# Performance work log

Hardware: AMD Instinct MI355X
Metric: run time of the kernel (lower is better)

## Reference

```python
import jax, jax.numpy as jnp
import numpy as np

B, S, D, H, DH, F = 2, 2048, 1024, 16, 64, 4096
K = 2048  # number of selected tokens (capacity_gamma=0.5 of B*S)
EPS = 1e-6
ROPE_THETA = 10000.0


def setup_inputs() -> dict:
    key = jax.random.key(0)
    ks = jax.random.split(key, 12)
    w = lambda k, shp: jax.random.normal(k, shp, dtype=jnp.float32) * 0.02
    # K unique flat indices into the B*S token grid (every other token -> unique, sorted)
    sel_flat = jnp.arange(K, dtype=jnp.int64) * 2
    return {
        "hidden_states": jax.random.normal(ks[0], (B, S, D), dtype=jnp.float32),
        "gating_signal": jax.random.uniform(ks[1], (B, S), dtype=jnp.float32),
        "sel_flat": sel_flat,
        "position_ids": jnp.tile(jnp.arange(S, dtype=jnp.int64), (B, 1)),
        "ln1_w": jnp.ones((D,), jnp.float32),
        "ln2_w": jnp.ones((D,), jnp.float32),
        "wq": w(ks[2], (D, H * DH)), "bq": jnp.zeros((H * DH,), jnp.float32),
        "wk": w(ks[3], (D, H * DH)), "bk": jnp.zeros((H * DH,), jnp.float32),
        "wv": w(ks[4], (D, H * DH)), "bv": jnp.zeros((H * DH,), jnp.float32),
        "wo": w(ks[5], (H * DH, D)),
        "w_gate": w(ks[6], (D, F)),
        "w_up": w(ks[7], (D, F)),
        "w_down": w(ks[8], (F, D)),
    }


def _rmsnorm(x, w):
    var = jnp.mean(jnp.square(x), axis=-1, keepdims=True)
    return x * jax.lax.rsqrt(var + EPS) * w


def _rope(x, pos):
    # x: [K, H, DH], pos: [K]
    half = DH // 2
    inv_freq = 1.0 / (ROPE_THETA ** (jnp.arange(half, dtype=jnp.float32) / half))
    ang = pos.astype(jnp.float32)[:, None] * inv_freq  # [K, half]
    cos = jnp.cos(ang)[:, None, :]
    sin = jnp.sin(ang)[:, None, :]
    x1, x2 = x[..., :half], x[..., half:]
    return jnp.concatenate([x1 * cos - x2 * sin, x2 * cos + x1 * sin], axis=-1)


def reference(hidden_states, gating_signal, sel_flat, position_ids,
              ln1_w, ln2_w, wq, bq, wk, bk, wv, bv, wo, w_gate, w_up, w_down):
    b_idx = sel_flat // S
    t_idx = sel_flat % S

    # --- gather selected tokens ---
    x = hidden_states[b_idx, t_idx]          # [K, D]
    g = gating_signal[b_idx, t_idx]          # [K]
    pos = position_ids[b_idx, t_idx]         # [K]

    # --- Qwen2 block on the selected tokens (single sequence of length K) ---
    h = _rmsnorm(x, ln1_w)
    q = _rope((h @ wq + bq).reshape(K, H, DH), pos)
    k = _rope((h @ wk + bk).reshape(K, H, DH), pos)
    v = (h @ wv + bv).reshape(K, H, DH)

    scores = jnp.einsum("qhd,khd->hqk", q, k) / np.sqrt(DH)  # [H, K, K]
    causal = jnp.tril(jnp.ones((K, K), dtype=bool))
    scores = jnp.where(causal, scores, jnp.finfo(scores.dtype).min)
    probs = jax.nn.softmax(scores, axis=-1)
    attn = jnp.einsum("hqk,khd->qhd", probs, v).reshape(K, H * DH) @ wo

    x1 = x + attn
    h2 = _rmsnorm(x1, ln2_w)
    mlp = (jax.nn.silu(h2 @ w_gate) * (h2 @ w_up)) @ w_down
    y = x1 + mlp                              # processed tokens [K, D]

    # --- gated residual scatter-back ---
    updated = x + (y - x) * g[:, None]
    return hidden_states.at[b_idx, t_idx].set(updated)
```

## Files before the change

### kernel.cpp

```cpp
#include <hip/hip_runtime.h>
#include <hip/hip_bf16.h>
#include <stdint.h>

#define K_TOK 2048
#define D_DIM 1024
#define H_N   16
#define DH_N  64
#define F_DIM 4096
#define S_SEQ 2048

typedef __attribute__((ext_vector_type(4))) float f32x4;
typedef __attribute__((ext_vector_type(8))) short bf16x8;

__device__ __forceinline__ float bf2f(ushort u) {
  union { unsigned u; float f; } c; c.u = ((unsigned)u) << 16; return c.f;
}
__device__ __forceinline__ ushort f2bf(float f) {
  union { float f; unsigned u; } c; c.f = f;
  unsigned x = c.u + 0x7fffu + ((c.u >> 16) & 1u);
  return (ushort)(x >> 16);
}

#define GLOAD_LDS16(GP, LP)                                                   \
  __builtin_amdgcn_global_load_lds(                                           \
      (const __attribute__((address_space(1))) unsigned int*)(GP),            \
      (__attribute__((address_space(3))) unsigned int*)(LP), 16, 0, 0)

__global__ __launch_bounds__(256) void prep_all(
    const float* __restrict__ wq, const float* __restrict__ wk,
    const float* __restrict__ wv, const float* __restrict__ wo,
    const float* __restrict__ wg, const float* __restrict__ wu,
    const float* __restrict__ wd, const float* __restrict__ bq,
    const float* __restrict__ bk, const float* __restrict__ bv,
    ushort* __restrict__ qkvT, ushort* __restrict__ woT,
    ushort* __restrict__ guT, ushort* __restrict__ wdT,
    float* __restrict__ biasqkv) {
  __shared__ float tile[64][65];
  int b = blockIdx.x;
  if (b >= 4096) {
    int i = (b - 4096) * 256 + threadIdx.x;
    if (i < 3072)
      biasqkv[i] = (i < 1024) ? bq[i] : (i < 2048 ? bk[i - 1024] : bv[i - 2048]);
    return;
  }
  const float* src;
  ushort* dst;
  int C, mul, add, ldd, tid_tile;
  if (b < 1024) {
    int seg = b >> 8; tid_tile = b & 255; C = 1024; mul = 1; add = 0; ldd = 1024;
    if (seg == 0) { src = wq; dst = qkvT; }
    else if (seg == 1) { src = wk; dst = qkvT + 1024 * 1024; }
    else if (seg == 2) { src = wv; dst = qkvT + 2048 * 1024; }
    else { src = wo; dst = woT; }
  } else if (b < 2048) { src = wg; dst = guT; tid_tile = b - 1024; C = 4096; mul = 2; add = 0; ldd = 1024; }
  else if (b < 3072) { src = wu; dst = guT; tid_tile = b - 2048; C = 4096; mul = 2; add = 1; ldd = 1024; }
  else { src = wd; dst = wdT; tid_tile = b - 3072; C = 1024; mul = 1; add = 0; ldd = 4096; }

  int nbx = C >> 6;
  int bx = tid_tile % nbx, by = tid_tile / nbx;
  int c0 = bx << 6, r0 = by << 6;
  int tx = threadIdx.x & 15, ty = threadIdx.x >> 4;
#pragma unroll
  for (int i = 0; i < 4; ++i) {
    float4 v = *(const float4*)&src[(size_t)(r0 + ty + i * 16) * C + c0 + tx * 4];
    *(float4*)&tile[ty + i * 16][tx * 4] = v;
  }
  __syncthreads();
#pragma unroll
  for (int i = 0; i < 4; ++i) {
    int c = ty + i * 16;
    ushort4 o;
    o.x = f2bf(tile[tx * 4 + 0][c]);
    o.y = f2bf(tile[tx * 4 + 1][c]);
    o.z = f2bf(tile[tx * 4 + 2][c]);
    o.w = f2bf(tile[tx * 4 + 3][c]);
    *(ushort4*)&dst[(size_t)((c0 + c) * mul + add) * ldd + r0 + tx * 4] = o;
  }
}

__global__ __launch_bounds__(256) void gather_copy(
    const float* __restrict__ hs, const float* __restrict__ gating,
    const int* __restrict__ sel32, const int* __restrict__ pos32,
    const float* __restrict__ w, float* __restrict__ outc,
    float* __restrict__ xbuf, ushort* __restrict__ hbuf,
    float* __restrict__ gbuf, int* __restrict__ rowb, int* __restrict__ rowt,
    int* __restrict__ rowpos) {
  __shared__ float red[4];
  int tid = threadIdx.x;
  if (blockIdx.x < 4096) {
    int idx = blockIdx.x * 256 + tid;
    ((float4*)outc)[idx] = ((const float4*)hs)[idx];
    return;
  }
  int i = blockIdx.x - 4096;
  bool is64 = (sel32[1] == 0 && sel32[3] == 0 && sel32[5] == 0);
  int sel = is64 ? sel32[2 * i] : sel32[i];
  int b = sel >> 11;
  int t = sel & 2047;
  const float4* src = (const float4*)(hs + ((size_t)b * S_SEQ + t) * D_DIM);
  float4 v = src[tid];
  float ss = v.x * v.x + v.y * v.y + v.z * v.z + v.w * v.w;
  for (int off = 32; off; off >>= 1) ss += __shfl_xor(ss, off);
  if ((tid & 63) == 0) red[tid >> 6] = ss;
  __syncthreads();
  float tot = red[0] + red[1] + red[2] + red[3];
  float rms = rsqrtf(tot * (1.f / 1024.f) + 1e-6f);
  ((float4*)(xbuf + (size_t)i * D_DIM))[tid] = v;
  float4 lw = ((const float4*)w)[tid];
  ushort4 hv;
  hv.x = f2bf(v.x * rms * lw.x); hv.y = f2bf(v.y * rms * lw.y);
  hv.z = f2bf(v.z * rms * lw.z); hv.w = f2bf(v.w * rms * lw.w);
  *(ushort4*)&hbuf[(size_t)i * D_DIM + tid * 4] = hv;
  if (tid == 0) {
    rowb[i] = b; rowt[i] = t;
    bool is64p = (pos32[1] == 0 && pos32[3] == 0 && pos32[5] == 0);
    int pidx = b * S_SEQ + t;
    rowpos[i] = is64p ? pos32[2 * pidx] : pos32[pidx];
    gbuf[i] = gating[pidx];
  }
}

__global__ __launch_bounds__(256) void rmsnorm_ep1(const float* __restrict__ xbuf,
                                                   const float* __restrict__ pb,
                                                   const float* __restrict__ w,
                                                   float* __restrict__ x1out,
                                                   ushort* __restrict__ h2out) {
  int i = blockIdx.x, tid = threadIdx.x;
  __shared__ float red[4];
  size_t e = (size_t)i * D_DIM;
  float4 v = ((const float4*)(xbuf + e))[tid];
  float4 p0 = ((const float4*)(pb + e))[tid];
  float4 p1 = ((const float4*)(pb + 2097152 + e))[tid];
  v.x += p0.x + p1.x; v.y += p0.y + p1.y; v.z += p0.z + p1.z; v.w += p0.w + p1.w;
  ((float4*)(x1out + e))[tid] = v;
  float ss = v.x * v.x + v.y * v.y + v.z * v.z + v.w * v.w;
  for (int off = 32; off; off >>= 1) ss += __shfl_xor(ss, off);
  if ((tid & 63) == 0) red[tid >> 6] = ss;
  __syncthreads();
  float tot = red[0] + red[1] + red[2] + red[3];
  float rms = rsqrtf(tot * (1.f / 1024.f) + 1e-6f);
  float4 lw = ((const float4*)w)[tid];
  ushort4 hv;
  hv.x = f2bf(v.x * rms * lw.x); hv.y = f2bf(v.y * rms * lw.y);
  hv.z = f2bf(v.z * rms * lw.z); hv.w = f2bf(v.w * rms * lw.w);
  *(ushort4*)&h2out[e + tid * 4] = hv;
}

__global__ __launch_bounds__(256) void ep3_k(const float* __restrict__ pb,
                                             const float* __restrict__ x1b,
                                             const float* __restrict__ xbuf,
                                             const float* __restrict__ gbuf,
                                             const int* __restrict__ rowb,
                                             const int* __restrict__ rowt,
                                             float* __restrict__ out) {
  int idx = blockIdx.x * 256 + threadIdx.x;
  int row = idx >> 8, c4 = idx & 255;
  size_t e = (size_t)row * D_DIM + c4 * 4;
  float4 s0 = *(const float4*)(pb + e);
  float4 s1 = *(const float4*)(pb + 2097152 + e);
  float4 s2 = *(const float4*)(pb + 2 * 2097152 + e);
  float4 s3 = *(const float4*)(pb + 3 * 2097152 + e);
  float4 x = *(const float4*)(xbuf + e);
  float4 x1 = *(const float4*)(x1b + e);
  float g = gbuf[row];
  float4 r;
  r.x = x.x + (x1.x + s0.x + s1.x + s2.x + s3.x - x.x) * g;
  r.y = x.y + (x1.y + s0.y + s1.y + s2.y + s3.y - x.y) * g;
  r.z = x.z + (x1.z + s0.z + s1.z + s2.z + s3.z - x.z) * g;
  r.w = x.w + (x1.w + s0.w + s1.w + s2.w + s3.w - x.w) * g;
  *(float4*)(out + ((size_t)rowb[row] * S_SEQ + rowt[row]) * D_DIM + c4 * 4) = r;
}

template <int MODE>
__global__ __launch_bounds__(256) void gemm_bt(
    const ushort* __restrict__ A, const ushort* __restrict__ BT,
    int M, int N, int ldk, int kdeff, int per,
    const float* __restrict__ bias,
    ushort* __restrict__ outb, float* __restrict__ outf) {
  __shared__ ushort lA[2][128 * 64];
  __shared__ ushort lB[2][128 * 64];
  int tid = threadIdx.x;
  int lane = tid & 63, wid = tid >> 6;
  int kidx = blockIdx.x / per;
  int bid = blockIdx.x % per;
  int nbn = N >> 7;
  int tm = bid / nbn, tn = bid % nbn;
  int wr = wid >> 1, wc = wid & 1;
  f32x4 acc[4][4];
#pragma unroll
  for (int m = 0; m < 4; ++m)
#pragma unroll
    for (int n = 0; n < 4; ++n) acc[m][n] = (f32x4){0.f, 0.f, 0.f, 0.f};

  const ushort* Ab = A + (size_t)(tm * 128) * ldk + (size_t)kidx * kdeff;
  const ushort* Bb = BT + (size_t)(tn * 128) * ldk + (size_t)kidx * kdeff;
  int lr = lane & 15, lg = lane >> 4;
  int prow = lane >> 3;
  int pch = lane & 7;
  int nk = kdeff >> 6;

  auto STG = [&](int bi, int t) {
#pragma unroll
    for (int p = 0; p < 4; ++p) {
      int rb = p * 32 + wid * 8;
      int row = rb + prow;
      int g = pch ^ (row & 7);
      GLOAD_LDS16(Ab + (size_t)row * ldk + t * 64 + g * 8, &lA[bi][rb * 64]);
      GLOAD_LDS16(Bb + (size_t)row * ldk + t * 64 + g * 8, &lB[bi][rb * 64]);
    }
  };

  STG(0, 0);
  STG(1, 1);
  asm volatile("s_waitcnt vmcnt(8)" ::: "memory");
  __builtin_amdgcn_s_barrier();

  for (int t = 0; t < nk; ++t) {
    int c = t & 1;
    const char* bA = (const char*)&lA[c][0];
    const char* bB = (const char*)&lB[c][0];
    bf16x8 bfv[4][2], af[4];
#pragma unroll
    for (int n = 0; n < 4; ++n) {
      int row = wc * 64 + n * 16 + lr;
#pragma unroll
      for (int kk = 0; kk < 2; ++kk)
        bfv[n][kk] = *(const bf16x8*)(bB + row * 128 + ((kk * 64 + lg * 16) ^ ((row & 7) << 4)));
    }
#pragma unroll
    for (int m = 0; m < 4; ++m) {
      int row = wr * 64 + m * 16 + lr;
      af[m] = *(const bf16x8*)(bA + row * 128 + ((lg * 16) ^ ((row & 7) << 4)));
    }
    __builtin_amdgcn_s_setprio(1);
#pragma unroll
    for (int m = 0; m < 4; ++m)
#pragma unroll
      for (int n = 0; n < 4; ++n)
        acc[m][n] = __builtin_amdgcn_mfma_f32_16x16x32_bf16(af[m], bfv[n][0], acc[m][n], 0, 0, 0);
    __builtin_amdgcn_s_setprio(0);
#pragma unroll
    for (int m = 0; m < 4; ++m) {
      int row = wr * 64 + m * 16 + lr;
      af[m] = *(const bf16x8*)(bA + row * 128 + ((64 + lg * 16) ^ ((row & 7) << 4)));
    }
    asm volatile("s_waitcnt lgkmcnt(0)" ::: "memory");
    __builtin_amdgcn_s_barrier();
    if (t + 2 < nk) STG(c, t + 2);
    __builtin_amdgcn_sched_barrier(0);
    __builtin_amdgcn_s_setprio(1);
#pragma unroll
    for (int m = 0; m < 4; ++m)
#pragma unroll
      for (int n = 0; n < 4; ++n)
        acc[m][n] = __builtin_amdgcn_mfma_f32_16x16x32_bf16(af[m], bfv[n][1], acc[m][n], 0, 0, 0);
    __builtin_amdgcn_s_setprio(0);
    if (t < nk - 1) {
      if (t + 2 < nk)
        asm volatile("s_waitcnt vmcnt(8)" ::: "memory");
      else
        asm volatile("s_waitcnt vmcnt(0)" ::: "memory");
      __builtin_amdgcn_s_barrier();
    }
  }

#pragma unroll
  for (int m = 0; m < 4; ++m) {
#pragma unroll
    for (int n = 0; n < 4; ++n) {
#pragma unroll
      for (int r = 0; r < 4; ++r) {
        int gr = tm * 128 + wr * 64 + m * 16 + lg * 4 + r;
        int gc = tn * 128 + wc * 64 + n * 16 + lr;
        float val = acc[m][n][r];
        if (MODE == 0) {
          outb[(size_t)gr * N + gc] = f2bf(val + bias[gc]);
        } else {
          outf[((size_t)kidx * M + gr) * N + gc] = val;
        }
      }
    }
  }
}

__global__ __launch_bounds__(512, 2) void gemm256_gu(const ushort* __restrict__ A,
                                                     const ushort* __restrict__ BT,
                                                     ushort* __restrict__ outb) {
  __shared__ ushort lA[2][256 * 64];
  __shared__ ushort lB[2][256 * 64];
  int tid = threadIdx.x, lane = tid & 63, wid = tid >> 6;
  int bid = blockIdx.x;
  int tn = (bid & 7) * 4 + ((bid >> 3) & 3);
  int tm = bid >> 5;
  int wm = wid >> 2, wn = wid & 3;
  int lr = lane & 15, lg = lane >> 4;
  const ushort* Ab = A + (size_t)(tm * 256) * 1024;
  const ushort* Bb = BT + (size_t)(tn * 256) * 1024;

  f32x4 acc[8][4];
#pragma unroll
  for (int m = 0; m < 8; ++m)
#pragma unroll
    for (int n = 0; n < 4; ++n) acc[m][n] = (f32x4){0.f, 0.f, 0.f, 0.f};

  int grow = lane >> 3;
  int gsw = (lane & 7) ^ grow;

  auto STG = [&](int bi, int t) {
#pragma unroll
    for (int r = 0; r < 4; ++r) {
      int rb = wid * 4 + r;
      int row = rb * 8 + grow;
      GLOAD_LDS16(Ab + (size_t)row * 1024 + t * 64 + gsw * 8, &lA[bi][rb * 512]);
      GLOAD_LDS16(Bb + (size_t)row * 1024 + t * 64 + gsw * 8, &lB[bi][rb * 512]);
    }
  };

  STG(0, 0);
  STG(1, 1);
  asm volatile("s_waitcnt vmcnt(8)" ::: "memory");
  __builtin_amdgcn_s_barrier();

  for (int t = 0; t < 16; ++t) {
    int c = t & 1;
    const char* bA = (const char*)&lA[c][0];
    const char* bB = (const char*)&lB[c][0];
    bf16x8 bfr[4][2], afh[4][2];
#pragma unroll
    for (int n = 0; n < 4; ++n) {
      int row = wn * 64 + n * 16 + lr;
#pragma unroll
      for (int kk = 0; kk < 2; ++kk)
        bfr[n][kk] = *(const bf16x8*)(bB + row * 128 + ((kk * 64 + lg * 16) ^ ((lr & 7) << 4)));
    }
#pragma unroll
    for (int m = 0; m < 4; ++m) {
      int row = wm * 128 + m * 16 + lr;
#pragma unroll
      for (int kk = 0; kk < 2; ++kk)
        afh[m][kk] = *(const bf16x8*)(bA + row * 128 + ((kk * 64 + lg * 16) ^ ((lr & 7) << 4)));
    }
    __builtin_amdgcn_s_setprio(1);
#pragma unroll
    for (int m = 0; m < 4; ++m)
#pragma unroll
      for (int n = 0; n < 4; ++n)
#pragma unroll
        for (int kk = 0; kk < 2; ++kk)
          acc[m][n] = __builtin_amdgcn_mfma_f32_16x16x32_bf16(afh[m][kk], bfr[n][kk],
                                                              acc[m][n], 0, 0, 0);
    __builtin_amdgcn_s_setprio(0);
#pragma unroll
    for (int m = 0; m < 4; ++m) {
      int row = wm * 128 + 64 + m * 16 + lr;
#pragma unroll
      for (int kk = 0; kk < 2; ++kk)
        afh[m][kk] = *(const bf16x8*)(bA + row * 128 + ((kk * 64 + lg * 16) ^ ((lr & 7) << 4)));
    }
    asm volatile("s_waitcnt lgkmcnt(0)" ::: "memory");
    __builtin_amdgcn_s_barrier();
    if (t + 2 < 16) STG(c, t + 2);
    __builtin_amdgcn_sched_barrier(0);
    __builtin_amdgcn_s_setprio(1);
#pragma unroll
    for (int m = 0; m < 4; ++m)
#pragma unroll
      for (int n = 0; n < 4; ++n)
#pragma unroll
        for (int kk = 0; kk < 2; ++kk)
          acc[4 + m][n] = __builtin_amdgcn_mfma_f32_16x16x32_bf16(afh[m][kk], bfr[n][kk],
                                                                  acc[4 + m][n], 0, 0, 0);
    __builtin_amdgcn_s_setprio(0);
    if (t < 15) {
      if (t + 2 < 16)
        asm volatile("s_waitcnt vmcnt(8)" ::: "memory");
      else
        asm volatile("s_waitcnt vmcnt(0)" ::: "memory");
      __builtin_amdgcn_s_barrier();
    }
  }

#pragma unroll
  for (int m = 0; m < 8; ++m) {
#pragma unroll
    for (int n = 0; n < 4; ++n) {
#pragma unroll
      for (int r = 0; r < 4; ++r) {
        int gr = tm * 256 + wm * 128 + m * 16 + lg * 4 + r;
        int gc = tn * 256 + wn * 64 + n * 16 + lr;
        float val = acc[m][n][r];
        float other = __shfl_xor(val, 1);
        if (!(lane & 1)) {
          float g = val, u = other;
          float a = g / (1.f + __expf(-g)) * u;
          outb[(size_t)gr * (F_DIM) + (gc >> 1)] = f2bf(a);
        }
      }
    }
  }
}

__global__ __launch_bounds__(256) void rope_vtrans(const ushort* __restrict__ qkv,
                                                   const int* __restrict__ rowpos,
                                                   ushort* __restrict__ qr,
                                                   ushort* __restrict__ kr,
                                                   ushort* __restrict__ vt) {
  __shared__ ushort tile[32][33];
  if (blockIdx.x < 4096) {
    int idx = blockIdx.x * 256 + threadIdx.x;
    int i = idx >> 9;
    int rem = idx & 511;
    int h = rem >> 5, d = rem & 31;
    float pos = (float)rowpos[i];
    float inv = __expf(-(float)d * (9.210340371976184f / 32.0f));
    float ang = pos * inv;
    float sn, cs;
    __sincosf(ang, &sn, &cs);
    size_t base = (size_t)i * 3072;
    float q1 = bf2f(qkv[base + h * 64 + d]);
    float q2 = bf2f(qkv[base + h * 64 + 32 + d]);
    float k1 = bf2f(qkv[base + 1024 + h * 64 + d]);
    float k2 = bf2f(qkv[base + 1024 + h * 64 + 32 + d]);
    size_t ob = ((size_t)h * K_TOK + i) * DH_N;
    qr[ob + d] = f2bf((q1 * cs - q2 * sn) * 0.125f);
    qr[ob + 32 + d] = f2bf((q2 * cs + q1 * sn) * 0.125f);
    kr[ob + d] = f2bf(k1 * cs - k2 * sn);
    kr[ob + 32 + d] = f2bf(k2 * cs + k1 * sn);
    return;
  }
  int bid = blockIdx.x - 4096;
  int bx = bid & 63, by = bid >> 6;
  int i0 = bx << 5, c0 = by << 5;
  int tx = threadIdx.x & 31, ty = threadIdx.x >> 5;
#pragma unroll
  for (int j = 0; j < 32; j += 8)
    tile[ty + j][tx] = qkv[(size_t)(i0 + ty + j) * 3072 + 2048 + c0 + tx];
  __syncthreads();
#pragma unroll
  for (int j = 0; j < 32; j += 8)
    vt[(size_t)(c0 + ty + j) * K_TOK + i0 + tx] = tile[tx][ty + j];
}

__global__ __launch_bounds__(256) void attn_mfma(const ushort* __restrict__ qr,
                                                 const ushort* __restrict__ kr,
                                                 const ushort* __restrict__ vt,
                                                 ushort* __restrict__ ows,
                                                 float* __restrict__ mlws) {
  __shared__ ushort ktile[2][64 * 64];
  __shared__ ushort vtile[2][64 * 64];
  __shared__ ushort pbuf[4][16 * 64];
  int tid = threadIdx.x, lane = tid & 63, wid = tid >> 6;
  int bid = blockIdx.x;
  int h = bid / 144;
  int rem = 143 - (bid % 144);
  int g = 0;
  while (rem >= 2 * (g + 1) * (g + 2)) ++g;
  int rem2 = rem - 2 * g * (g + 1);
  int qt = (g << 2) + rem2 / (g + 1);
  int ci = rem2 % (g + 1);
  int slot = h * 144 + rem;
  int q0 = qt << 6;
  int t0 = ci << 2;
  int t1 = min(t0 + 3, qt);

  const ushort* Kh = kr + (size_t)h * K_TOK * DH_N;
  const ushort* Vh = vt + (size_t)h * DH_N * K_TOK;
  int lr = lane & 15, lg = lane >> 4;
  int qbase = q0 + wid * 16;

  bf16x8 qf[2];
  const ushort* Qp = qr + ((size_t)h * K_TOK + qbase + lr) * DH_N + lg * 8;
  qf[0] = *(const bf16x8*)(Qp);
  qf[1] = *(const bf16x8*)(Qp + 32);

  f32x4 oa[4];
  float mreg[4], lreg[4];
#pragma unroll
  for (int ct = 0; ct < 4; ++ct) oa[ct] = (f32x4){0.f, 0.f, 0.f, 0.f};
#pragma unroll
  for (int r = 0; r < 4; ++r) { mreg[r] = -1e30f; lreg[r] = 0.f; }

  char* pws = (char*)&pbuf[wid][0];
  int srow8 = lane >> 3, schunk = lane & 7;

  auto stage = [&](int bi, int kb) {
#pragma unroll
    for (int j = 0; j < 2; ++j) {
      int rbase = wid * 16 + j * 8;
      int row = rbase + srow8;
      int gch = schunk ^ (row & 7);
      GLOAD_LDS16(Kh + (size_t)(kb + row) * DH_N + gch * 8, &ktile[bi][rbase * 64]);
      GLOAD_LDS16(Vh + (size_t)row * K_TOK + kb + gch * 8, &vtile[bi][rbase * 64]);
    }
  };

  stage(0, t0 << 6);
  int cur = 0;
  for (int t = t0; t <= t1; ++t) {
    int kb = t << 6;
    __syncthreads();
    if (t < t1) stage(cur ^ 1, (t + 1) << 6);

    const char* kt = (const char*)&ktile[cur][0];
    const char* vtl = (const char*)&vtile[cur][0];

    f32x4 sa[4];
#pragma unroll
    for (int ct = 0; ct < 4; ++ct) sa[ct] = (f32x4){0.f, 0.f, 0.f, 0.f};
#pragma unroll
    for (int s = 0; s < 2; ++s) {
#pragma unroll
      for (int ct = 0; ct < 4; ++ct) {
        int row = ct * 16 + lr;
        bf16x8 kf = *(const bf16x8*)(kt + row * 128 + ((s * 64 + lg * 16) ^ ((row & 7) << 4)));
        sa[ct] = __builtin_amdgcn_mfma_f32_16x16x32_bf16(qf[s], kf, sa[ct], 0, 0, 0);
      }
    }

#pragma unroll
    for (int r = 0; r < 4; ++r) {
      int q = qbase + lg * 4 + r;
      int prow = lg * 4 + r;
      float sv[4];
      float mx = mreg[r];
#pragma unroll
      for (int ct = 0; ct < 4; ++ct) {
        int key = kb + ct * 16 + lr;
        float x = sa[ct][r];
        sv[ct] = (key <= q) ? x : -1e30f;
        mx = fmaxf(mx, sv[ct]);
      }
      mx = fmaxf(mx, __shfl_xor(mx, 1));
      mx = fmaxf(mx, __shfl_xor(mx, 2));
      mx = fmaxf(mx, __shfl_xor(mx, 4));
      mx = fmaxf(mx, __shfl_xor(mx, 8));
      float resc = __expf(mreg[r] - mx);
      float ps = 0.f;
#pragma unroll
      for (int ct = 0; ct < 4; ++ct) {
        float p = __expf(sv[ct] - mx);
        ps += p;
        *(ushort*)(pws + prow * 128 + ((ct * 32 + lr * 2) ^ ((prow & 7) << 4))) = f2bf(p);
      }
      ps += __shfl_xor(ps, 1);
      ps += __shfl_xor(ps, 2);
      ps += __shfl_xor(ps, 4);
      ps += __shfl_xor(ps, 8);
      lreg[r] = lreg[r] * resc + ps;
      mreg[r] = mx;
#pragma unroll
      for (int ct = 0; ct < 4; ++ct) oa[ct][r] *= resc;
    }

    bf16x8 pf[2];
#pragma unroll
    for (int s = 0; s < 2; ++s)
      pf[s] = *(const bf16x8*)(pws + lr * 128 + ((s * 64 + lg * 16) ^ ((lr & 7) << 4)));
#pragma unroll
    for (int s = 0; s < 2; ++s) {
#pragma unroll
      for (int ct = 0; ct < 4; ++ct) {
        int row = ct * 16 + lr;
        bf16x8 vf = *(const bf16x8*)(vtl + row * 128 + ((s * 64 + lg * 16) ^ ((row & 7) << 4)));
        oa[ct] = __builtin_amdgcn_mfma_f32_16x16x32_bf16(pf[s], vf, oa[ct], 0, 0, 0);
      }
    }
    cur ^= 1;
  }

#pragma unroll
  for (int ct = 0; ct < 4; ++ct) {
#pragma unroll
    for (int r = 0; r < 4; ++r) {
      int prow = wid * 16 + lg * 4 + r;
      ows[(size_t)slot * 4096 + prow * 64 + ct * 16 + lr] = f2bf(oa[ct][r]);
    }
  }
  if (lr == 0) {
#pragma unroll
    for (int r = 0; r < 4; ++r) {
      int prow = wid * 16 + lg * 4 + r;
      mlws[(size_t)slot * 128 + prow] = mreg[r];
      mlws[(size_t)slot * 128 + 64 + prow] = lreg[r];
    }
  }
}

__global__ __launch_bounds__(256) void attn_combine(const ushort* __restrict__ ows,
                                                    const float* __restrict__ mlws,
                                                    ushort* __restrict__ aout) {
  int bid = blockIdx.x;
  int h = bid & 15, qt = bid >> 4;
  int g = qt >> 2;
  int nc = g + 1;
  int base = h * 144 + 2 * g * (g + 1) + (qt & 3) * nc;
  int tid = threadIdx.x;
  int row = tid >> 2, c0 = (tid & 3) * 16;
  float M = -1e30f;
  for (int i = 0; i < nc; ++i)
    M = fmaxf(M, mlws[(size_t)(base + i) * 128 + row]);
  float L = 0.f;
  float acc[16];
#pragma unroll
  for (int j = 0; j < 16; ++j) acc[j] = 0.f;
  for (int i = 0; i < nc; ++i) {
    size_t sl = (size_t)(base + i);
    float w = __expf(mlws[sl * 128 + row] - M);
    L += mlws[sl * 128 + 64 + row] * w;
    const bf16x8* op = (const bf16x8*)(ows + sl * 4096 + row * 64 + c0);
    bf16x8 v0 = op[0], v1 = op[1];
#pragma unroll
    for (int j = 0; j < 8; ++j) acc[j] += bf2f(((ushort)v0[j])) * w;
#pragma unroll
    for (int j = 0; j < 8; ++j) acc[8 + j] += bf2f(((ushort)v1[j])) * w;
  }
  float inv = 1.f / L;
  int q = qt * 64 + row;
  ushort* dst = aout + (size_t)q * D_DIM + h * DH_N + c0;
#pragma unroll
  for (int j = 0; j < 16; ++j) dst[j] = f2bf(acc[j] * inv);
}

extern "C" void kernel_launch(void* const* d_in, const int* in_sizes, int n_in,
                              void* d_out, int out_size, void* d_ws, size_t ws_size,
                              hipStream_t stream) {
  const float* hs = (const float*)d_in[0];
  const float* gating = (const float*)d_in[1];
  const int* sel32 = (const int*)d_in[2];
  const int* pos32 = (const int*)d_in[3];
  const float* ln1w = (const float*)d_in[4];
  const float* ln2w = (const float*)d_in[5];
  const float* wq = (const float*)d_in[6];
  const float* bq = (const float*)d_in[7];
  const float* wk = (const float*)d_in[8];
  const float* bk = (const float*)d_in[9];
  const float* wv = (const float*)d_in[10];
  const float* bv = (const float*)d_in[11];
  const float* wo = (const float*)d_in[12];
  const float* wg = (const float*)d_in[13];
  const float* wu = (const float*)d_in[14];
  const float* wd = (const float*)d_in[15];
  float* out = (float*)d_out;

  char* wsb = (char*)d_ws;
  size_t off = 0;
  auto alloc = [&](size_t bytes) -> void* {
    void* p = wsb + off;
    off += (bytes + 255) & ~(size_t)255;
    return p;
  };
  ushort* qkvT = (ushort*)alloc(3072ull * 1024 * 2);
  ushort* woT = (ushort*)alloc(1024ull * 1024 * 2);
  ushort* guT = (ushort*)alloc(8192ull * 1024 * 2);
  ushort* wdT = (ushort*)alloc(1024ull * 4096 * 2);
  float* biasqkv = (float*)alloc(3072 * 4);
  float* xbuf = (float*)alloc(2048ull * 1024 * 4);
  ushort* hbuf = (ushort*)alloc(2048ull * 1024 * 2);
  ushort* qkv = (ushort*)alloc(2048ull * 3072 * 2);
  ushort* qrb = (ushort*)alloc(16ull * 2048 * 64 * 2);
  ushort* krb = (ushort*)alloc(16ull * 2048 * 64 * 2);
  ushort* vtb = (ushort*)alloc(16ull * 64 * 2048 * 2);
  ushort* aoutb = (ushort*)alloc(2048ull * 1024 * 2);
  float* pbuf = (float*)hbuf;
  float* x1b = (float*)alloc(2048ull * 1024 * 4);
  ushort* h2b = (ushort*)alloc(2048ull * 1024 * 2);
  ushort* actb = (ushort*)alloc(2048ull * 4096 * 2);
  ushort* aows = (ushort*)x1b;
  float* amlws = (float*)((char*)x1b + 2304ull * 4096 * 2);
  float* gbuf = (float*)alloc(2048 * 4);
  int* rowb = (int*)alloc(2048 * 4);
  int* rowt = (int*)alloc(2048 * 4);
  int* rowpos = (int*)alloc(2048 * 4);
  if (off > ws_size) return;

  prep_all<<<4108, 256, 0, stream>>>(wq, wk, wv, wo, wg, wu, wd, bq, bk, bv, qkvT, woT, guT,
                                     wdT, biasqkv);
  gather_copy<<<6144, 256, 0, stream>>>(hs, gating, sel32, pos32, ln1w, out, xbuf, hbuf, gbuf,
                                        rowb, rowt, rowpos);
  gemm_bt<0><<<16 * 24, 256, 0, stream>>>(hbuf, qkvT, 2048, 3072, 1024, 1024, 16 * 24, biasqkv,
                                          qkv, nullptr);
  rope_vtrans<<<6144, 256, 0, stream>>>(qkv, rowpos, qrb, krb, vtb);
  attn_mfma<<<16 * 144, 256, 0, stream>>>(qrb, krb, vtb, aows, amlws);
  attn_combine<<<512, 256, 0, stream>>>(aows, amlws, aoutb);
  gemm_bt<4><<<2 * 16 * 8, 256, 0, stream>>>(aoutb, woT, 2048, 1024, 1024, 512, 16 * 8, nullptr,
                                             nullptr, pbuf);
  rmsnorm_ep1<<<2048, 256, 0, stream>>>(xbuf, pbuf, ln2w, x1b, h2b);
  gemm256_gu<<<256, 512, 0, stream>>>(h2b, guT, actb);
  gemm_bt<4><<<4 * 16 * 8, 256, 0, stream>>>(actb, wdT, 2048, 1024, 4096, 1024, 16 * 8, nullptr,
                                             nullptr, pbuf);
  ep3_k<<<2048, 256, 0, stream>>>(pbuf, x1b, xbuf, gbuf, rowb, rowt, out);
}
```

Measured before the change: 194.9 us.

## Switch gate/up GEMM to triple-buffered K=32 stages with packed LDS layout

The fused gate/up GEMM previously staged K=64 slices in two LDS buffers. It now stages K=32 slices in three buffers, packing two matrix rows per 128-byte LDS row with an XOR swizzle. Loads are issued two stages ahead, with an extra barrier pair per iteration. This uses less LDS per stage and adds pipeline depth, but doubles the loop iterations and barrier count and issues fewer MFMAs per synchronisation.

New measurement: 206.1 us. 5.7% more time.

```diff
diff --git a/kernel.cpp b/kernel.cpp
--- a/kernel.cpp
+++ b/kernel.cpp
@@ -286,8 +286,8 @@
 __global__ __launch_bounds__(512, 2) void gemm256_gu(const ushort* __restrict__ A,
                                                      const ushort* __restrict__ BT,
                                                      ushort* __restrict__ outb) {
-  __shared__ ushort lA[2][256 * 64];
-  __shared__ ushort lB[2][256 * 64];
+  __shared__ ushort lA[3][128 * 64];
+  __shared__ ushort lB[3][128 * 64];
   int tid = threadIdx.x, lane = tid & 63, wid = tid >> 6;
   int bid = blockIdx.x;
   int tn = (bid & 7) * 4 + ((bid >> 3) & 3);
@@ -303,81 +303,66 @@
 #pragma unroll
     for (int n = 0; n < 4; ++n) acc[m][n] = (f32x4){0.f, 0.f, 0.f, 0.f};
 
-  int grow = lane >> 3;
-  int gsw = (lane & 7) ^ grow;
+  int sR0 = wid * 8 + (lane >> 3);
+  int scp = lane & 7;
 
   auto STG = [&](int bi, int t) {
 #pragma unroll
-    for (int r = 0; r < 4; ++r) {
-      int rb = wid * 4 + r;
-      int row = rb * 8 + grow;
-      GLOAD_LDS16(Ab + (size_t)row * 1024 + t * 64 + gsw * 8, &lA[bi][rb * 512]);
-      GLOAD_LDS16(Bb + (size_t)row * 1024 + t * 64 + gsw * 8, &lB[bi][rb * 512]);
+    for (int j = 0; j < 2; ++j) {
+      int R = j * 64 + sR0;
+      int c = scp ^ (R & 7);
+      int grow = 2 * R + (c >> 2);
+      int kch = c & 3;
+      GLOAD_LDS16(Ab + (size_t)grow * 1024 + t * 32 + kch * 8, &lA[bi][(j * 64 + wid * 8) * 64]);
+      GLOAD_LDS16(Bb + (size_t)grow * 1024 + t * 32 + kch * 8, &lB[bi][(j * 64 + wid * 8) * 64]);
     }
   };
 
   STG(0, 0);
   STG(1, 1);
+  STG(2, 2);
   asm volatile("s_waitcnt vmcnt(8)" ::: "memory");
   __builtin_amdgcn_s_barrier();
 
-  for (int t = 0; t < 16; ++t) {
-    int c = t & 1;
-    const char* bA = (const char*)&lA[c][0];
-    const char* bB = (const char*)&lB[c][0];
-    bf16x8 bfr[4][2], afh[4][2];
+  for (int t = 0; t < 32; ++t) {
+    if (t > 0) {
+      __builtin_amdgcn_s_barrier();
+      __builtin_amdgcn_sched_barrier(0);
+      if (t + 2 < 32) {
+        STG((t + 2) % 3, t + 2);
+        asm volatile("s_waitcnt vmcnt(8)" ::: "memory");
+      } else if (t + 1 < 32) {
+        asm volatile("s_waitcnt vmcnt(4)" ::: "memory");
+      } else {
+        asm volatile("s_waitcnt vmcnt(0)" ::: "memory");
+      }
+      __builtin_amdgcn_s_barrier();
+      __builtin_amdgcn_sched_barrier(0);
+    }
+    const char* bA = (const char*)&lA[t % 3][0];
+    const char* bB = (const char*)&lB[t % 3][0];
+    bf16x8 bf[4], af[8];
 #pragma unroll
     for (int n = 0; n < 4; ++n) {
-      int row = wn * 64 + n * 16 + lr;
-#pragma unroll
-      for (int kk = 0; kk < 2; ++kk)
-        bfr[n][kk] = *(const bf16x8*)(bB + row * 128 + ((kk * 64 + lg * 16) ^ ((lr & 7) << 4)));
-    }
-#pragma unroll
-    for (int m = 0; m < 4; ++m) {
-      int row = wm * 128 + m * 16 + lr;
-#pragma unroll
-      for (int kk = 0; kk < 2; ++kk)
-        afh[m][kk] = *(const bf16x8*)(bA + row * 128 + ((kk * 64 + lg * 16) ^ ((lr & 7) << 4)));
+      int rho = wn * 64 + n * 16 + lr;
+      int R = rho >> 1;
+      int cc = ((rho & 1) * 4 + lg) ^ (R & 7);
+      bf[n] = *(const bf16x8*)(bB + R * 128 + cc * 16);
+    }
+#pragma unroll
+    for (int m = 0; m < 8; ++m) {
+      int rho = wm * 128 + m * 16 + lr;
+      int R = rho >> 1;
+      int cc = ((rho & 1) * 4 + lg) ^ (R & 7);
+      af[m] = *(const bf16x8*)(bA + R * 128 + cc * 16);
     }
     __builtin_amdgcn_s_setprio(1);
 #pragma unroll
-    for (int m = 0; m < 4; ++m)
+    for (int m = 0; m < 8; ++m)
 #pragma unroll
       for (int n = 0; n < 4; ++n)
-#pragma unroll
-        for (int kk = 0; kk < 2; ++kk)
-          acc[m][n] = __builtin_amdgcn_mfma_f32_16x16x32_bf16(afh[m][kk], bfr[n][kk],
-                                                              acc[m][n], 0, 0, 0);
+        acc[m][n] = __builtin_amdgcn_mfma_f32_16x16x32_bf16(af[m], bf[n], acc[m][n], 0, 0, 0);
     __builtin_amdgcn_s_setprio(0);
-#pragma unroll
-    for (int m = 0; m < 4; ++m) {
-      int row = wm * 128 + 64 + m * 16 + lr;
-#pragma unroll
-      for (int kk = 0; kk < 2; ++kk)
-        afh[m][kk] = *(const bf16x8*)(bA + row * 128 + ((kk * 64 + lg * 16) ^ ((lr & 7) << 4)));
-    }
-    asm volatile("s_waitcnt lgkmcnt(0)" ::: "memory");
-    __builtin_amdgcn_s_barrier();
-    if (t + 2 < 16) STG(c, t + 2);
-    __builtin_amdgcn_sched_barrier(0);
-    __builtin_amdgcn_s_setprio(1);
-#pragma unroll
-    for (int m = 0; m < 4; ++m)
-#pragma unroll
-      for (int n = 0; n < 4; ++n)
-#pragma unroll
-        for (int kk = 0; kk < 2; ++kk)
-          acc[4 + m][n] = __builtin_amdgcn_mfma_f32_16x16x32_bf16(afh[m][kk], bfr[n][kk],
-                                                                  acc[4 + m][n], 0, 0, 0);
-    __builtin_amdgcn_s_setprio(0);
-    if (t < 15) {
-      if (t + 2 < 16)
-        asm volatile("s_waitcnt vmcnt(8)" ::: "memory");
-      else
-        asm volatile("s_waitcnt vmcnt(0)" ::: "memory");
-      __builtin_amdgcn_s_barrier();
-    }
   }
 
 #pragma unroll
```

## Restructure gate-up GEMM into 8-wave ping-pong phases with split-K half tiles

Applied to the files above, without the earlier changes.

Rewrites the main loop of the fused gate/up GEMM kernel. Each 64-wide K tile now splits into two 32-wide halves, each stored in its own LDS buffer with a new paired-row XOR swizzle. Each iteration runs four barrier-separated phases, and the global->LDS loads for the next tile (A half, then B half) are interleaved between MFMA clusters. The aim is finer-grained overlap of loads with MFMA, in the style of a ping-pong schedule, plus fewer registers held for fragments. The cost is more barriers per iteration and a new swizzle layout that has to stay correct.

After: 202.5 us. 3.9% more time.

```diff
diff --git a/kernel.cpp b/kernel.cpp
--- a/kernel.cpp
+++ b/kernel.cpp
@@ -286,8 +286,8 @@
 __global__ __launch_bounds__(512, 2) void gemm256_gu(const ushort* __restrict__ A,
                                                      const ushort* __restrict__ BT,
                                                      ushort* __restrict__ outb) {
-  __shared__ ushort lA[2][256 * 64];
-  __shared__ ushort lB[2][256 * 64];
+  __shared__ ushort lA[2][2][128 * 64];
+  __shared__ ushort lB[2][2][128 * 64];
   int tid = threadIdx.x, lane = tid & 63, wid = tid >> 6;
   int bid = blockIdx.x;
   int tn = (bid & 7) * 4 + ((bid >> 3) & 3);
@@ -303,82 +303,142 @@
 #pragma unroll
     for (int n = 0; n < 4; ++n) acc[m][n] = (f32x4){0.f, 0.f, 0.f, 0.f};
 
-  int grow = lane >> 3;
-  int gsw = (lane & 7) ^ grow;
-
-  auto STG = [&](int bi, int t) {
-#pragma unroll
-    for (int r = 0; r < 4; ++r) {
-      int rb = wid * 4 + r;
-      int row = rb * 8 + grow;
-      GLOAD_LDS16(Ab + (size_t)row * 1024 + t * 64 + gsw * 8, &lA[bi][rb * 512]);
-      GLOAD_LDS16(Bb + (size_t)row * 1024 + t * 64 + gsw * 8, &lB[bi][rb * 512]);
+  int sR = lane >> 3;
+  int scp = lane & 7;
+
+  auto STG_A = [&](int buf, int t, int kk) {
+#pragma unroll
+    for (int j = 0; j < 2; ++j) {
+      int R = j * 64 + wid * 8 + sR;
+      int c = scp ^ (R & 7);
+      int grow = 2 * R + (c >> 2);
+      GLOAD_LDS16(Ab + (size_t)grow * 1024 + t * 64 + kk * 32 + (c & 3) * 8,
+                  &lA[buf][kk][(j * 64 + wid * 8) * 64]);
     }
   };
-
-  STG(0, 0);
-  STG(1, 1);
-  asm volatile("s_waitcnt vmcnt(8)" ::: "memory");
-  __builtin_amdgcn_s_barrier();
+  auto STG_B = [&](int buf, int t, int kk) {
+#pragma unroll
+    for (int j = 0; j < 2; ++j) {
+      int R = j * 64 + wid * 8 + sR;
+      int c = scp ^ (R & 7);
+      int grow = 2 * R + (c >> 2);
+      GLOAD_LDS16(Bb + (size_t)grow * 1024 + t * 64 + kk * 32 + (c & 3) * 8,
+                  &lB[buf][kk][(j * 64 + wid * 8) * 64]);
+    }
+  };
+
+#define PH_BAR() { __builtin_amdgcn_s_barrier(); __builtin_amdgcn_sched_barrier(0); }
+
+  STG_A(0, 0, 0); STG_B(0, 0, 0);
+  STG_A(0, 0, 1); STG_B(0, 0, 1);
+  asm volatile("s_waitcnt vmcnt(4)" ::: "memory");
+  PH_BAR();
 
   for (int t = 0; t < 16; ++t) {
-    int c = t & 1;
-    const char* bA = (const char*)&lA[c][0];
-    const char* bB = (const char*)&lB[c][0];
-    bf16x8 bfr[4][2], afh[4][2];
+    int c = t & 1, o = c ^ 1;
+    const char* a0 = (const char*)&lA[c][0][0];
+    const char* a1 = (const char*)&lA[c][1][0];
+    const char* b0 = (const char*)&lB[c][0][0];
+    const char* b1 = (const char*)&lB[c][1][0];
+    bf16x8 bf[4], af[4];
+
 #pragma unroll
     for (int n = 0; n < 4; ++n) {
-      int row = wn * 64 + n * 16 + lr;
-#pragma unroll
-      for (int kk = 0; kk < 2; ++kk)
-        bfr[n][kk] = *(const bf16x8*)(bB + row * 128 + ((kk * 64 + lg * 16) ^ ((lr & 7) << 4)));
+      int rho = wn * 64 + n * 16 + lr; int R = rho >> 1;
+      int cc = (((rho & 1) << 2) | lg) ^ (R & 7);
+      bf[n] = *(const bf16x8*)(b0 + R * 128 + cc * 16);
     }
 #pragma unroll
     for (int m = 0; m < 4; ++m) {
-      int row = wm * 128 + m * 16 + lr;
-#pragma unroll
-      for (int kk = 0; kk < 2; ++kk)
-        afh[m][kk] = *(const bf16x8*)(bA + row * 128 + ((kk * 64 + lg * 16) ^ ((lr & 7) << 4)));
-    }
-    __builtin_amdgcn_s_setprio(1);
-#pragma unroll
-    for (int m = 0; m < 4; ++m)
-#pragma unroll
-      for (int n = 0; n < 4; ++n)
-#pragma unroll
-        for (int kk = 0; kk < 2; ++kk)
-          acc[m][n] = __builtin_amdgcn_mfma_f32_16x16x32_bf16(afh[m][kk], bfr[n][kk],
-                                                              acc[m][n], 0, 0, 0);
-    __builtin_amdgcn_s_setprio(0);
-#pragma unroll
-    for (int m = 0; m < 4; ++m) {
-      int row = wm * 128 + 64 + m * 16 + lr;
-#pragma unroll
-      for (int kk = 0; kk < 2; ++kk)
-        afh[m][kk] = *(const bf16x8*)(bA + row * 128 + ((kk * 64 + lg * 16) ^ ((lr & 7) << 4)));
-    }
+      int rho = wm * 128 + m * 16 + lr; int R = rho >> 1;
+      int cc = (((rho & 1) << 2) | lg) ^ (R & 7);
+      af[m] = *(const bf16x8*)(a0 + R * 128 + cc * 16);
+    }
+    if (t + 1 < 16) STG_A(o, t + 1, 0);
+    PH_BAR();
     asm volatile("s_waitcnt lgkmcnt(0)" ::: "memory");
-    __builtin_amdgcn_s_barrier();
-    if (t + 2 < 16) STG(c, t + 2);
     __builtin_amdgcn_sched_barrier(0);
     __builtin_amdgcn_s_setprio(1);
 #pragma unroll
     for (int m = 0; m < 4; ++m)
 #pragma unroll
       for (int n = 0; n < 4; ++n)
-#pragma unroll
-        for (int kk = 0; kk < 2; ++kk)
-          acc[4 + m][n] = __builtin_amdgcn_mfma_f32_16x16x32_bf16(afh[m][kk], bfr[n][kk],
-                                                                  acc[4 + m][n], 0, 0, 0);
+        acc[m][n] = __builtin_amdgcn_mfma_f32_16x16x32_bf16(af[m], bf[n], acc[m][n], 0, 0, 0);
     __builtin_amdgcn_s_setprio(0);
-    if (t < 15) {
-      if (t + 2 < 16)
-        asm volatile("s_waitcnt vmcnt(8)" ::: "memory");
-      else
-        asm volatile("s_waitcnt vmcnt(0)" ::: "memory");
-      __builtin_amdgcn_s_barrier();
-    }
-  }
+    PH_BAR();
+
+#pragma unroll
+    for (int m = 0; m < 4; ++m) {
+      int rho = wm * 128 + 64 + m * 16 + lr; int R = rho >> 1;
+      int cc = (((rho & 1) << 2) | lg) ^ (R & 7);
+      af[m] = *(const bf16x8*)(a0 + R * 128 + cc * 16);
+    }
+    if (t + 1 < 16) {
+      STG_B(o, t + 1, 0);
+      asm volatile("s_waitcnt vmcnt(4)" ::: "memory");
+    } else {
+      asm volatile("s_waitcnt vmcnt(0)" ::: "memory");
+    }
+    PH_BAR();
+    asm volatile("s_waitcnt lgkmcnt(0)" ::: "memory");
+    __builtin_amdgcn_sched_barrier(0);
+    __builtin_amdgcn_s_setprio(1);
+#pragma unroll
+    for (int m = 0; m < 4; ++m)
+#pragma unroll
+      for (int n = 0; n < 4; ++n)
+        acc[4 + m][n] = __builtin_amdgcn_mfma_f32_16x16x32_bf16(af[m], bf[n], acc[4 + m][n], 0, 0, 0);
+    __builtin_amdgcn_s_setprio(0);
+    PH_BAR();
+
+#pragma unroll
+    for (int n = 0; n < 4; ++n) {
+      int rho = wn * 64 + n * 16 + lr; int R = rho >> 1;
+      int cc = (((rho & 1) << 2) | lg) ^ (R & 7);
+      bf[n] = *(const bf16x8*)(b1 + R * 128 + cc * 16);
+    }
+#pragma unroll
+    for (int m = 0; m < 4; ++m) {
+      int rho = wm * 128 + m * 16 + lr; int R = rho >> 1;
+      int cc = (((rho & 1) << 2) | lg) ^ (R & 7);
+      af[m] = *(const bf16x8*)(a1 + R * 128 + cc * 16);
+    }
+    if (t + 1 < 16) STG_A(o, t + 1, 1);
+    PH_BAR();
+    asm volatile("s_waitcnt lgkmcnt(0)" ::: "memory");
+    __builtin_amdgcn_sched_barrier(0);
+    __builtin_amdgcn_s_setprio(1);
+#pragma unroll
+    for (int m = 0; m < 4; ++m)
+#pragma unroll
+      for (int n = 0; n < 4; ++n)
+        acc[m][n] = __builtin_amdgcn_mfma_f32_16x16x32_bf16(af[m], bf[n], acc[m][n], 0, 0, 0);
+    __builtin_amdgcn_s_setprio(0);
+    PH_BAR();
+
+#pragma unroll
+    for (int m = 0; m < 4; ++m) {
+      int rho = wm * 128 + 64 + m * 16 + lr; int R = rho >> 1;
+      int cc = (((rho & 1) << 2) | lg) ^ (R & 7);
+      af[m] = *(const bf16x8*)(a1 + R * 128 + cc * 16);
+    }
+    if (t + 1 < 16) {
+      STG_B(o, t + 1, 1);
+      asm volatile("s_waitcnt vmcnt(4)" ::: "memory");
+    }
+    PH_BAR();
+    asm volatile("s_waitcnt lgkmcnt(0)" ::: "memory");
+    __builtin_amdgcn_sched_barrier(0);
+    __builtin_amdgcn_s_setprio(1);
+#pragma unroll
+    for (int m = 0; m < 4; ++m)
+#pragma unroll
+      for (int n = 0; n < 4; ++n)
+        acc[4 + m][n] = __builtin_amdgcn_mfma_f32_16x16x32_bf16(af[m], bf[n], acc[4 + m][n], 0, 0, 0);
+    __builtin_amdgcn_s_setprio(0);
+    PH_BAR();
+  }
+#undef PH_BAR
 
 #pragma unroll
   for (int m = 0; m < 8; ++m) {
```
